# Performance work log

Measured on AMD Instinct MI355X. Metric: run time of the kernel, lower is better.

The kernel has to match this reference:

```python
import jax, jax.numpy as jnp
import numpy as np
from jax import lax

SUB_NO, E_NO, I_NO, T_NO, HID_NO = 20, 2000, 500, 50, 10
SH = SUB_NO * HID_NO
B, T_DATA = 8, 5000


def setup_inputs() -> dict:
    key = jax.random.key(0)
    ks = jax.random.split(key, 8)
    return {
        "S_e": jax.random.uniform(ks[0], (B, T_DATA, E_NO), dtype=jnp.float32),
        "S_i": jax.random.uniform(ks[1], (B, T_DATA, I_NO), dtype=jnp.float32),
        "C_syn_e": jax.random.normal(ks[2], (SUB_NO, E_NO), dtype=jnp.float32) * 0.1,
        "C_syn_i": jax.random.normal(ks[3], (SUB_NO, I_NO), dtype=jnp.float32) * 0.1,
        "E_scale": jnp.zeros((E_NO,), jnp.float32),
        "I_scale": jnp.zeros((I_NO,), jnp.float32),
        "W_e_layer1": jax.random.normal(ks[4], (SH, T_NO), dtype=jnp.float32) * 0.01,
        "W_layer2": jnp.full((SUB_NO, HID_NO), -1.0, jnp.float32),
        "b_layer1": jnp.zeros((SH,), jnp.float32),
        "W_hist": jax.random.normal(ks[5], (SH, T_NO), dtype=jnp.float32) * 0.01,
        "W_sub": jnp.zeros((SUB_NO,), jnp.float32),
        "V_o": jnp.zeros((1,), jnp.float32),
    }


def _forward(S_e, C_syn_e, E_scale, W_e_layer1, W_layer2, b_layer1, W_hist, V_o):
    Bx, T, _ = S_e.shape
    sub_no = C_syn_e.shape[0]
    T_no = W_e_layer1.shape[1]
    hid_no = W_e_layer1.shape[0] // sub_no
    sh = sub_no * hid_no

    Se = S_e * jnp.exp(E_scale)[None, None, :]
    syn_e = jnp.einsum("bte,se->bst", Se, C_syn_e)  # [B, sub, T]

    # torch F.conv1d(groups=sub_no) with left zero-pad of T_no-1 and flipped kernel
    w = jnp.flip(W_e_layer1, axis=1)[:, None, :]  # [SH, 1, T_no]
    conv = lax.conv_general_dilated(
        syn_e, w, window_strides=(1,), padding=[(T_no - 1, 0)],
        dimension_numbers=("NCH", "OIH", "NCH"), feature_group_count=sub_no,
    )  # [B, SH, T]

    hist_kern = jnp.flip(W_hist, axis=1).T  # [T_no, SH]; row T_no-1 multiplies most recent step
    conv_seq = jnp.moveaxis(conv, 2, 0)  # [T, B, SH]
    init_win = jnp.zeros((Bx, T_no, sh), S_e.dtype)

    def step(window, conv_t):
        hist_in = jnp.einsum("btc,tc->bc", window, hist_kern)
        new = jnp.tanh(hist_in + conv_t + b_layer1)
        window = jnp.concatenate([window[:, 1:], new[:, None]], axis=1)
        return window, new

    _, ys = lax.scan(step, init_win, conv_seq)  # [T, B, SH]
    ys = jnp.moveaxis(ys, 0, 1).reshape(Bx, T, sub_no, hid_no)

    # 1x1 grouped conv == per-subunit weighted sum over hidden channels
    sub_out = jnp.einsum("btsh,sh->bts", ys, jnp.exp(W_layer2))
    return jnp.sum(sub_out, axis=-1) + V_o[0]  # [B, T]


def reference(S_e, S_i, C_syn_e, C_syn_i, E_scale, I_scale, W_e_layer1,
              W_layer2, b_layer1, W_hist, W_sub, V_o):
    # S_i, C_syn_i, I_scale, W_sub are unused in the original forward (E-only pathway)
    return _forward(S_e, C_syn_e, E_scale, W_e_layer1, W_layer2, b_layer1, W_hist, V_o)
```

## Files before the change

### kernel.cpp

```cpp
#include <hip/hip_runtime.h>
#include <utility>
#include <cstddef>

#define SUBN 20
#define EN   2000
#define TN   50
#define HIDN 10
#define CHN  200
#define BN   8
#define TD   5000
#define TP   5056
#define NOB  79

#define OFF_CP  0
#define OFF_G   40000
#define OFF_SYN 40200
#define OFF_U   849160
#define OFF_Y   8938760

__global__ __launch_bounds__(256) void k_prep(const float* __restrict__ Ce,
                                              const float* __restrict__ Es,
                                              const float* __restrict__ W2,
                                              float* __restrict__ Cp,
                                              float* __restrict__ g) {
    int idx = blockIdx.x * 256 + threadIdx.x;
    if (idx < SUBN * EN) {
        int e = idx % EN;
        Cp[idx] = Ce[idx] * __expf(Es[e]);
    } else if (idx < SUBN * EN + CHN) {
        g[idx - SUBN * EN] = __expf(W2[idx - SUBN * EN]);
    }
}

__device__ __forceinline__ float wred(float x) {
    x += __int_as_float(__builtin_amdgcn_update_dpp(0, __float_as_int(x), 0x111, 0xF, 0xF, true));
    x += __int_as_float(__builtin_amdgcn_update_dpp(0, __float_as_int(x), 0x112, 0xF, 0xF, true));
    x += __int_as_float(__builtin_amdgcn_update_dpp(0, __float_as_int(x), 0x114, 0xF, 0xF, true));
    x += __int_as_float(__builtin_amdgcn_update_dpp(0, __float_as_int(x), 0x118, 0xF, 0xF, true));
    x += __int_as_float(__builtin_amdgcn_update_dpp(0, __float_as_int(x), 0x142, 0xF, 0xF, true));
    x += __int_as_float(__builtin_amdgcn_update_dpp(0, __float_as_int(x), 0x143, 0xF, 0xF, true));
    return x;
}

__global__ __launch_bounds__(256, 2) void k_gemm(const float* __restrict__ Se,
                                                 const float* __restrict__ Cp,
                                                 float* __restrict__ syn) {
    const int tid  = threadIdx.x;
    const int lane = tid & 63;
    const int wave = tid >> 6;
    const int r0   = blockIdx.x * 32 + wave * 8;
    const size_t rbase = (size_t)r0 * EN;
    const int le   = 4 * lane;
    const bool ok7 = (le < 208);

    float acc[SUBN][8];
    #pragma unroll
    for (int s = 0; s < SUBN; ++s)
        #pragma unroll
        for (int t = 0; t < 8; ++t) acc[s][t] = 0.0f;

    for (int k = 0; k < 8; ++k) {
        int coff = 256 * k + le;
        if (k == 7 && !ok7) coff = 0;
        float4 se[8];
        #pragma unroll
        for (int t = 0; t < 8; ++t)
            se[t] = *(const float4*)(Se + rbase + (size_t)t * EN + coff);
        if (k == 7 && !ok7) {
            #pragma unroll
            for (int t = 0; t < 8; ++t) se[t] = make_float4(0.f, 0.f, 0.f, 0.f);
        }
        const float* cp0 = Cp + 256 * k + le;
        #pragma unroll
        for (int s = 0; s < SUBN; ++s) {
            float4 cv = *(const float4*)(cp0 + s * EN);
            #pragma unroll
            for (int t = 0; t < 8; ++t) {
                acc[s][t] = fmaf(cv.x, se[t].x, acc[s][t]);
                acc[s][t] = fmaf(cv.y, se[t].y, acc[s][t]);
                acc[s][t] = fmaf(cv.z, se[t].z, acc[s][t]);
                acc[s][t] = fmaf(cv.w, se[t].w, acc[s][t]);
            }
        }
    }

    #pragma unroll
    for (int s = 0; s < SUBN; ++s)
        #pragma unroll
        for (int t = 0; t < 8; ++t) acc[s][t] = wred(acc[s][t]);

    if (lane == 63) {
        #pragma unroll
        for (int t = 0; t < 8; ++t) {
            int r  = r0 + t;
            int b  = r / TD;
            int tt = r - b * TD;
            float* sp = syn + (size_t)(b * SUBN) * TP + tt;
            #pragma unroll
            for (int s = 0; s < SUBN; ++s) sp[(size_t)s * TP] = acc[s][t];
        }
    }
}

__global__ __launch_bounds__(256, 4) void k_conv(const float* __restrict__ syn,
                                                 const float* __restrict__ W1,
                                                 const float* __restrict__ b1,
                                                 float* __restrict__ u) {
    __shared__ __align__(16) float srow[52 + TP + 12];
    const int bs  = blockIdx.x / HIDN;
    const int h   = blockIdx.x % HIDN;
    const int s   = bs % SUBN;
    const int tid = threadIdx.x;

    for (int i = tid; i < 13; i += 256) ((float4*)srow)[i] = make_float4(0,0,0,0);
    for (int i = tid; i < 3; i += 256)
        ((float4*)(srow + 52 + TP))[i] = make_float4(0,0,0,0);
    const float4* srcp = (const float4*)(syn + (size_t)bs * TP);
    for (int i = tid; i < TP / 4; i += 256) ((float4*)(srow + 52))[i] = srcp[i];

    const int c = s * HIDN + h;
    float wreg[TN];
    #pragma unroll
    for (int j = 0; j < TN; ++j) wreg[j] = W1[c * TN + j];
    const float bh = b1[c];
    __syncthreads();

    float* urow = u + (size_t)(bs * HIDN + h) * TP;
    for (int task = 0; task < 3; ++task) {
        int gidx = tid + task * 256;
        if (gidx >= 723) break;
        int t0 = gidx * 7;
        float a[7];
        #pragma unroll
        for (int m = 0; m < 7; ++m) a[m] = bh;
        #pragma unroll
        for (int kk = 0; kk < 56; ++kk) {
            int k = kk - 49;
            float xv = srow[52 + t0 + k];
            #pragma unroll
            for (int m = 0; m < 7; ++m) {
                int j = m - k;
                if (j >= 0 && j < TN) a[m] = fmaf(wreg[j], xv, a[m]);
            }
        }
        #pragma unroll
        for (int m = 0; m < 7; ++m) {
            int t = t0 + m;
            if (t < TP) urow[t] = a[m];
        }
    }
}

struct Rec {
    float wl[64];
    float wn1, wn2, wn3, wn4, wn5, wn6;
    float acc0, acc1, acc2, acc3;
    float pend[8];
    float yv[8];
    float4 upipe[8];
    float4 cur;
    float bval;
    const float* urow;
    float* yrow8;
    int lane16;
    int tbase;
    bool m0, m1, m2, storer;
};

template<int P>
__device__ __forceinline__ void rec_step(Rec& S) {
    if constexpr ((P & 3) == 0) {
        constexpr int Q = (P >> 2) & 7;
        S.cur = S.upipe[Q];
        int tl = S.tbase + P + 32;
        if (tl > TP - 4) tl = TP - 4;
        S.upipe[Q] = *(const float4*)(&S.urow[tl]);
    }
    float uval;
    if constexpr ((P & 3) == 0) uval = S.cur.x;
    else if constexpr ((P & 3) == 1) uval = S.cur.y;
    else if constexpr ((P & 3) == 2) uval = S.cur.z;
    else uval = S.cur.w;

    float pre = S.pend[P & 7] + uval;
    float ex = __builtin_amdgcn_exp2f(pre * 2.8853900817779268f);
    float rc = __builtin_amdgcn_rcpf(ex + 1.0f);
    float y  = __builtin_fmaf(-2.0f, rc, 1.0f);
    S.yv[P & 7] = y;

    S.acc0 = __builtin_fmaf(S.wl[( 64 - P) & 63], y, S.acc0);
    S.acc1 = __builtin_fmaf(S.wl[( 80 - P) & 63], y, S.acc1);
    S.acc2 = __builtin_fmaf(S.wl[( 96 - P) & 63], y, S.acc2);
    S.acc3 = __builtin_fmaf(S.wl[(112 - P) & 63], y, S.acc3);

    S.pend[(P + 6) & 7] = __builtin_fmaf(S.wn6, y, S.bval);
    S.pend[(P + 1) & 7] = __builtin_fmaf(S.wn1, y, S.pend[(P + 1) & 7]);
    S.pend[(P + 2) & 7] = __builtin_fmaf(S.wn2, y, S.pend[(P + 2) & 7]);
    S.pend[(P + 3) & 7] = __builtin_fmaf(S.wn3, y, S.pend[(P + 3) & 7]);
    S.pend[(P + 4) & 7] = __builtin_fmaf(S.wn4, y, S.pend[(P + 4) & 7]);
    S.pend[(P + 5) & 7] = __builtin_fmaf(S.wn5, y, S.pend[(P + 5) & 7]);

    constexpr int SB  = (P + 7) & 63;
    constexpr int KB  = SB >> 4;
    constexpr int OWB = SB & 15;
    float av;
    if constexpr (KB == 0) av = S.acc0;
    else if constexpr (KB == 1) av = S.acc1;
    else if constexpr (KB == 2) av = S.acc2;
    else av = S.acc3;
    S.bval = __int_as_float(
        __builtin_amdgcn_ds_swizzle(__float_as_int(av), (OWB << 5) | 0x10));
    float nv = (S.lane16 == OWB) ? 0.0f : av;
    if constexpr (KB == 0) S.acc0 = nv;
    else if constexpr (KB == 1) S.acc1 = nv;
    else if constexpr (KB == 2) S.acc2 = nv;
    else S.acc3 = nv;

    if constexpr ((P & 7) == 7) {
        float a0 = S.m0 ? S.yv[1] : S.yv[0];
        float a1 = S.m0 ? S.yv[3] : S.yv[2];
        float a2 = S.m0 ? S.yv[5] : S.yv[4];
        float a3 = S.m0 ? S.yv[7] : S.yv[6];
        float b0 = S.m1 ? a1 : a0;
        float b1 = S.m1 ? a3 : a2;
        float sv = S.m2 ? b1 : b0;
        if (S.storer) S.yrow8[S.tbase + P - 7] = sv;
    }
}

template<int... Ps>
__device__ __forceinline__ void rec_steps(Rec& S, std::integer_sequence<int, Ps...>) {
    (rec_step<Ps>(S), ...);
}

__global__ __launch_bounds__(256) void k_rec(const float* __restrict__ u,
                                             const float* __restrict__ Wh,
                                             float* __restrict__ ybuf) {
    const int tid   = blockIdx.x * 256 + threadIdx.x;
    const int group = tid >> 4;
    Rec S;
    S.lane16 = tid & 15;
    const int c = group % CHN;
    S.urow  = u    + (size_t)group * TP;
    S.yrow8 = ybuf + (size_t)group * TP + (S.lane16 & 7);
    S.m0 = (S.lane16 & 1) != 0;
    S.m1 = (S.lane16 & 2) != 0;
    S.m2 = (S.lane16 & 4) != 0;
    S.storer = S.lane16 < 8;
    const float* whc = Wh + c * TN;
    S.wn1 = whc[0]; S.wn2 = whc[1]; S.wn3 = whc[2];
    S.wn4 = whc[3]; S.wn5 = whc[4]; S.wn6 = whc[5];
    #pragma unroll
    for (int m = 0; m < 64; ++m) {
        int d = (S.lane16 + m) & 63;
        S.wl[m] = (d >= 7 && d <= TN) ? whc[d - 1] : 0.0f;
    }
    S.acc0 = S.acc1 = S.acc2 = S.acc3 = 0.f;
    #pragma unroll
    for (int i = 0; i < 8; ++i) S.pend[i] = 0.f;
    S.bval = 0.f;
    #pragma unroll
    for (int q = 0; q < 8; ++q) S.upipe[q] = *(const float4*)(&S.urow[4 * q]);

    for (int ob = 0; ob < NOB; ++ob) {
        S.tbase = ob * 64;
        rec_steps(S, std::make_integer_sequence<int, 64>{});
    }
}

__global__ __launch_bounds__(256) void k_out(const float* __restrict__ ybuf,
                                             const float* __restrict__ g,
                                             const float* __restrict__ Vo,
                                             float* __restrict__ out) {
    const int cchunk = blockIdx.x & 3;
    const int tb     = blockIdx.x >> 2;
    const int idx4   = tb * 256 + threadIdx.x;
    if (idx4 >= BN * TD / 4) return;
    const int t4 = idx4 * 4;
    const int b  = t4 / TD;
    const int tt = t4 - b * TD;
    const float* yp = ybuf + ((size_t)b * CHN + cchunk * 50) * TP + tt;
    const float* gp = g + cchunk * 50;
    float ax = 0.f, ay = 0.f, az = 0.f, aw = 0.f;
    if (cchunk == 0) { float v = Vo[0]; ax = ay = az = aw = v; }
    #pragma unroll 10
    for (int cc = 0; cc < 50; ++cc) {
        float4 y4 = *(const float4*)(yp + (size_t)cc * TP);
        float gc = gp[cc];
        ax = fmaf(gc, y4.x, ax);
        ay = fmaf(gc, y4.y, ay);
        az = fmaf(gc, y4.z, az);
        aw = fmaf(gc, y4.w, aw);
    }
    atomicAdd(out + t4 + 0, ax);
    atomicAdd(out + t4 + 1, ay);
    atomicAdd(out + t4 + 2, az);
    atomicAdd(out + t4 + 3, aw);
}

extern "C" void kernel_launch(void* const* d_in, const int* in_sizes, int n_in,
                              void* d_out, int out_size, void* d_ws, size_t ws_size,
                              hipStream_t stream) {
    const float* Se = (const float*)d_in[0];
    const float* Ce = (const float*)d_in[2];
    const float* Es = (const float*)d_in[4];
    const float* W1 = (const float*)d_in[6];
    const float* W2 = (const float*)d_in[7];
    const float* b1 = (const float*)d_in[8];
    const float* Wh = (const float*)d_in[9];
    const float* Vo = (const float*)d_in[11];
    float* ws  = (float*)d_ws;
    float* Cp  = ws + OFF_CP;
    float* g   = ws + OFF_G;
    float* syn = ws + OFF_SYN;
    float* u   = ws + OFF_U;
    float* yb  = ws + OFF_Y;
    float* out = (float*)d_out;

    hipMemsetAsync(d_out, 0, (size_t)out_size * sizeof(float), stream);
    hipLaunchKernelGGL(k_prep, dim3(158), dim3(256), 0, stream, Ce, Es, W2, Cp, g);
    hipLaunchKernelGGL(k_gemm, dim3(1250), dim3(256), 0, stream, Se, Cp, syn);
    hipLaunchKernelGGL(k_conv, dim3(BN * SUBN * HIDN), dim3(256), 0, stream, syn, W1, b1, u);
    hipLaunchKernelGGL(k_rec,  dim3(100), dim3(256), 0, stream, u, Wh, yb);
    hipLaunchKernelGGL(k_out,  dim3(160), dim3(256), 0, stream, yb, g, Vo, out);
}
```

Measured before the change: 880.1 us.

## Fold tanh scale into weights, shorten recurrence critical path, retile gemm and output

The 2*log2(e) tanh scale is pre-multiplied into the conv weights, bias and history weights, which removes one multiply from each recurrence step. The broadcast partial sum is now added to u off the dependency chain instead of seeding the pend FMA, and the lane reset uses a multiply by a mask. The GEMM now handles 4 rows per wave with software-prefetched Se and Cp loads and vector stores, and the output reduction is split into 10 channel chunks for more blocks. The changes trade extra registers and more atomics for a shorter serial path and more parallelism.

```diff
diff --git a/kernel.cpp b/kernel.cpp
--- a/kernel.cpp
+++ b/kernel.cpp
@@ -11,6 +11,7 @@
 #define TD   5000
 #define TP   5056
 #define NOB  79
+#define LAM  2.8853900817779268f
 
 #define OFF_CP  0
 #define OFF_G   40000
@@ -42,44 +43,58 @@
     return x;
 }
 
-__global__ __launch_bounds__(256, 2) void k_gemm(const float* __restrict__ Se,
-                                                 const float* __restrict__ Cp,
-                                                 float* __restrict__ syn) {
+__global__ __launch_bounds__(256) void k_gemm(const float* __restrict__ Se,
+                                              const float* __restrict__ Cp,
+                                              float* __restrict__ syn) {
     const int tid  = threadIdx.x;
     const int lane = tid & 63;
     const int wave = tid >> 6;
-    const int r0   = blockIdx.x * 32 + wave * 8;
+    const int r0   = blockIdx.x * 16 + wave * 4;
     const size_t rbase = (size_t)r0 * EN;
     const int le   = 4 * lane;
     const bool ok7 = (le < 208);
 
-    float acc[SUBN][8];
+    float acc[SUBN][4];
     #pragma unroll
     for (int s = 0; s < SUBN; ++s)
         #pragma unroll
-        for (int t = 0; t < 8; ++t) acc[s][t] = 0.0f;
+        for (int t = 0; t < 4; ++t) acc[s][t] = 0.0f;
+
+    float4 se_n[4];
+    #pragma unroll
+    for (int t = 0; t < 4; ++t)
+        se_n[t] = *(const float4*)(Se + rbase + (size_t)t * EN + le);
 
     for (int k = 0; k < 8; ++k) {
-        int coff = 256 * k + le;
-        if (k == 7 && !ok7) coff = 0;
-        float4 se[8];
-        #pragma unroll
-        for (int t = 0; t < 8; ++t)
-            se[t] = *(const float4*)(Se + rbase + (size_t)t * EN + coff);
+        float4 se_c[4];
+        #pragma unroll
+        for (int t = 0; t < 4; ++t) se_c[t] = se_n[t];
         if (k == 7 && !ok7) {
             #pragma unroll
-            for (int t = 0; t < 8; ++t) se[t] = make_float4(0.f, 0.f, 0.f, 0.f);
+            for (int t = 0; t < 4; ++t) se_c[t] = make_float4(0.f, 0.f, 0.f, 0.f);
+        }
+        if (k < 7) {
+            int kn   = k + 1;
+            int coff = 256 * kn + le;
+            if (kn == 7 && !ok7) coff = 0;
+            #pragma unroll
+            for (int t = 0; t < 4; ++t)
+                se_n[t] = *(const float4*)(Se + rbase + (size_t)t * EN + coff);
         }
         const float* cp0 = Cp + 256 * k + le;
+        float4 cvq[3];
+        #pragma unroll
+        for (int j = 0; j < 3; ++j) cvq[j] = *(const float4*)(cp0 + j * EN);
         #pragma unroll
         for (int s = 0; s < SUBN; ++s) {
-            float4 cv = *(const float4*)(cp0 + s * EN);
+            float4 cv = cvq[s % 3];
+            if (s + 3 < SUBN) cvq[s % 3] = *(const float4*)(cp0 + (s + 3) * EN);
             #pragma unroll
-            for (int t = 0; t < 8; ++t) {
-                acc[s][t] = fmaf(cv.x, se[t].x, acc[s][t]);
-                acc[s][t] = fmaf(cv.y, se[t].y, acc[s][t]);
-                acc[s][t] = fmaf(cv.z, se[t].z, acc[s][t]);
-                acc[s][t] = fmaf(cv.w, se[t].w, acc[s][t]);
+            for (int t = 0; t < 4; ++t) {
+                acc[s][t] = fmaf(cv.x, se_c[t].x, acc[s][t]);
+                acc[s][t] = fmaf(cv.y, se_c[t].y, acc[s][t]);
+                acc[s][t] = fmaf(cv.z, se_c[t].z, acc[s][t]);
+                acc[s][t] = fmaf(cv.w, se_c[t].w, acc[s][t]);
             }
         }
     }
@@ -87,18 +102,16 @@
     #pragma unroll
     for (int s = 0; s < SUBN; ++s)
         #pragma unroll
-        for (int t = 0; t < 8; ++t) acc[s][t] = wred(acc[s][t]);
+        for (int t = 0; t < 4; ++t) acc[s][t] = wred(acc[s][t]);
 
     if (lane == 63) {
-        #pragma unroll
-        for (int t = 0; t < 8; ++t) {
-            int r  = r0 + t;
-            int b  = r / TD;
-            int tt = r - b * TD;
-            float* sp = syn + (size_t)(b * SUBN) * TP + tt;
-            #pragma unroll
-            for (int s = 0; s < SUBN; ++s) sp[(size_t)s * TP] = acc[s][t];
-        }
+        const int b  = r0 / TD;
+        const int tt = r0 - b * TD;
+        float* sp = syn + (size_t)(b * SUBN) * TP + tt;
+        #pragma unroll
+        for (int s = 0; s < SUBN; ++s)
+            *(float4*)(sp + (size_t)s * TP) =
+                make_float4(acc[s][0], acc[s][1], acc[s][2], acc[s][3]);
     }
 }
 
@@ -121,8 +134,8 @@
     const int c = s * HIDN + h;
     float wreg[TN];
     #pragma unroll
-    for (int j = 0; j < TN; ++j) wreg[j] = W1[c * TN + j];
-    const float bh = b1[c];
+    for (int j = 0; j < TN; ++j) wreg[j] = LAM * W1[c * TN + j];
+    const float bh = LAM * b1[c];
     __syncthreads();
 
     float* urow = u + (size_t)(bs * HIDN + h) * TP;
@@ -153,13 +166,14 @@
 
 struct Rec {
     float wl[64];
+    float rst[16];
     float wn1, wn2, wn3, wn4, wn5, wn6;
     float acc0, acc1, acc2, acc3;
     float pend[8];
+    float bv[8];
     float yv[8];
     float4 upipe[8];
     float4 cur;
-    float bval;
     const float* urow;
     float* yrow8;
     int lane16;
@@ -182,10 +196,11 @@
     else if constexpr ((P & 3) == 2) uval = S.cur.z;
     else uval = S.cur.w;
 
-    float pre = S.pend[P & 7] + uval;
-    float ex = __builtin_amdgcn_exp2f(pre * 2.8853900817779268f);
-    float rc = __builtin_amdgcn_rcpf(ex + 1.0f);
-    float y  = __builtin_fmaf(-2.0f, rc, 1.0f);
+    float uc  = uval + S.bv[P & 7];
+    float pre = S.pend[P & 7] + uc;
+    float ex  = __builtin_amdgcn_exp2f(pre);
+    float rc  = __builtin_amdgcn_rcpf(ex + 1.0f);
+    float y   = __builtin_fmaf(-2.0f, rc, 1.0f);
     S.yv[P & 7] = y;
 
     S.acc0 = __builtin_fmaf(S.wl[( 64 - P) & 63], y, S.acc0);
@@ -193,7 +208,7 @@
     S.acc2 = __builtin_fmaf(S.wl[( 96 - P) & 63], y, S.acc2);
     S.acc3 = __builtin_fmaf(S.wl[(112 - P) & 63], y, S.acc3);
 
-    S.pend[(P + 6) & 7] = __builtin_fmaf(S.wn6, y, S.bval);
+    S.pend[(P + 6) & 7] = S.wn6 * y;
     S.pend[(P + 1) & 7] = __builtin_fmaf(S.wn1, y, S.pend[(P + 1) & 7]);
     S.pend[(P + 2) & 7] = __builtin_fmaf(S.wn2, y, S.pend[(P + 2) & 7]);
     S.pend[(P + 3) & 7] = __builtin_fmaf(S.wn3, y, S.pend[(P + 3) & 7]);
@@ -208,9 +223,9 @@
     else if constexpr (KB == 1) av = S.acc1;
     else if constexpr (KB == 2) av = S.acc2;
     else av = S.acc3;
-    S.bval = __int_as_float(
+    S.bv[(P + 7) & 7] = __int_as_float(
         __builtin_amdgcn_ds_swizzle(__float_as_int(av), (OWB << 5) | 0x10));
-    float nv = (S.lane16 == OWB) ? 0.0f : av;
+    float nv = av * S.rst[OWB];
     if constexpr (KB == 0) S.acc0 = nv;
     else if constexpr (KB == 1) S.acc1 = nv;
     else if constexpr (KB == 2) S.acc2 = nv;
@@ -248,17 +263,18 @@
     S.m2 = (S.lane16 & 4) != 0;
     S.storer = S.lane16 < 8;
     const float* whc = Wh + c * TN;
-    S.wn1 = whc[0]; S.wn2 = whc[1]; S.wn3 = whc[2];
-    S.wn4 = whc[3]; S.wn5 = whc[4]; S.wn6 = whc[5];
+    S.wn1 = LAM * whc[0]; S.wn2 = LAM * whc[1]; S.wn3 = LAM * whc[2];
+    S.wn4 = LAM * whc[3]; S.wn5 = LAM * whc[4]; S.wn6 = LAM * whc[5];
     #pragma unroll
     for (int m = 0; m < 64; ++m) {
         int d = (S.lane16 + m) & 63;
-        S.wl[m] = (d >= 7 && d <= TN) ? whc[d - 1] : 0.0f;
-    }
+        S.wl[m] = (d >= 7 && d <= TN) ? LAM * whc[d - 1] : 0.0f;
+    }
+    #pragma unroll
+    for (int m = 0; m < 16; ++m) S.rst[m] = (S.lane16 == m) ? 0.0f : 1.0f;
     S.acc0 = S.acc1 = S.acc2 = S.acc3 = 0.f;
     #pragma unroll
-    for (int i = 0; i < 8; ++i) S.pend[i] = 0.f;
-    S.bval = 0.f;
+    for (int i = 0; i < 8; ++i) { S.pend[i] = 0.f; S.bv[i] = 0.f; }
     #pragma unroll
     for (int q = 0; q < 8; ++q) S.upipe[q] = *(const float4*)(&S.urow[4 * q]);
 
@@ -272,19 +288,19 @@
                                              const float* __restrict__ g,
                                              const float* __restrict__ Vo,
                                              float* __restrict__ out) {
-    const int cchunk = blockIdx.x & 3;
-    const int tb     = blockIdx.x >> 2;
+    const int cchunk = blockIdx.x % 10;
+    const int tb     = blockIdx.x / 10;
     const int idx4   = tb * 256 + threadIdx.x;
     if (idx4 >= BN * TD / 4) return;
     const int t4 = idx4 * 4;
     const int b  = t4 / TD;
     const int tt = t4 - b * TD;
-    const float* yp = ybuf + ((size_t)b * CHN + cchunk * 50) * TP + tt;
-    const float* gp = g + cchunk * 50;
+    const float* yp = ybuf + ((size_t)b * CHN + cchunk * 20) * TP + tt;
+    const float* gp = g + cchunk * 20;
     float ax = 0.f, ay = 0.f, az = 0.f, aw = 0.f;
     if (cchunk == 0) { float v = Vo[0]; ax = ay = az = aw = v; }
-    #pragma unroll 10
-    for (int cc = 0; cc < 50; ++cc) {
+    #pragma unroll
+    for (int cc = 0; cc < 20; ++cc) {
         float4 y4 = *(const float4*)(yp + (size_t)cc * TP);
         float gc = gp[cc];
         ax = fmaf(gc, y4.x, ax);
@@ -319,8 +335,8 @@
 
     hipMemsetAsync(d_out, 0, (size_t)out_size * sizeof(float), stream);
     hipLaunchKernelGGL(k_prep, dim3(158), dim3(256), 0, stream, Ce, Es, W2, Cp, g);
-    hipLaunchKernelGGL(k_gemm, dim3(1250), dim3(256), 0, stream, Se, Cp, syn);
+    hipLaunchKernelGGL(k_gemm, dim3(2500), dim3(256), 0, stream, Se, Cp, syn);
     hipLaunchKernelGGL(k_conv, dim3(BN * SUBN * HIDN), dim3(256), 0, stream, syn, W1, b1, u);
     hipLaunchKernelGGL(k_rec,  dim3(100), dim3(256), 0, stream, u, Wh, yb);
-    hipLaunchKernelGGL(k_out,  dim3(160), dim3(256), 0, stream, yb, g, Vo, out);
-}
+    hipLaunchKernelGGL(k_out,  dim3(400), dim3(256), 0, stream, yb, g, Vo, out);
+}
```

Measured after the change: 1.045 ms. +18.8%, slower.
